# Performance work log

Hardware: AMD Instinct MI355X
Metric: run time of the kernel (lower is better)

The kernel has to match this reference:

```python
import jax, jax.numpy as jnp
import numpy as np
import math

S, B, H, NH, HD = 2048, 1, 4096, 32, 128
ROT = HD // 2  # 2D RoPE: each half of head_dim gets its own rotary embedding


def _rotate_half(x):
    x1, x2 = jnp.split(x, 2, axis=-1)
    return jnp.concatenate((-x2, x1), axis=-1)


def _rope_tables(max_pos, dim):
    inv_freq = 1.0 / (10000.0 ** (jnp.arange(0, dim, 2, dtype=jnp.float32) / dim))
    freqs = jnp.arange(max_pos, dtype=jnp.float32)[:, None] * inv_freq[None, :]  # [P, dim/2]
    emb = jnp.concatenate((freqs, freqs), axis=-1)  # [P, dim]
    return jnp.cos(emb), jnp.sin(emb)


def _apply_rope(q, k, cos_t, sin_t, pid):
    # q,k: [S,B,NH,ROT]; pid: [S,B]
    c = cos_t[pid][:, :, None, :]  # [S,B,1,ROT]
    s = sin_t[pid][:, :, None, :]
    return q * c + _rotate_half(q) * s, k * c + _rotate_half(k) * s


def setup_inputs() -> dict:
    key = jax.random.key(0)
    k1, k2, k3, k4, k5 = jax.random.split(key, 5)
    hidden_states = jax.random.normal(k1, (S, B, H), dtype=jnp.float32)
    pos = jnp.arange(S, dtype=jnp.int32)[None, :]          # [1,S] standard positions
    blk = jnp.zeros((1, S), dtype=jnp.int32)                # block positions (pre-gmask all zeros)
    position_ids = jnp.stack([pos, blk], axis=1)            # [B,2,S]
    # causal mask: True = masked out
    attention_mask = jnp.triu(jnp.ones((S, S), dtype=bool), k=1)[None, None]  # [B,1,S,S]
    Wqkv = jax.random.normal(k2, (3 * H, H), dtype=jnp.float32) * 0.02
    bqkv = jax.random.normal(k3, (3 * H,), dtype=jnp.float32) * 0.02
    Wd = jax.random.normal(k4, (H, H), dtype=jnp.float32) * 0.02
    bd = jax.random.normal(k5, (H,), dtype=jnp.float32) * 0.02
    return {"hidden_states": hidden_states, "position_ids": position_ids,
            "attention_mask": attention_mask, "layer_id": 5,
            "Wqkv": Wqkv, "bqkv": bqkv, "Wd": Wd, "bd": bd}


def reference(hidden_states, position_ids, attention_mask, layer_id, Wqkv, bqkv, Wd, bd):
    # QKV projection: [S,B,H] -> [S,B,NH,3*HD]
    mixed = hidden_states @ Wqkv.T + bqkv
    mixed = mixed.reshape(S, B, NH, 3 * HD)
    q, k, v = jnp.split(mixed, 3, axis=-1)  # each [S,B,NH,HD]

    # 2D rotary position embedding on the two head-dim halves
    q1, q2 = jnp.split(q, 2, axis=-1)
    k1, k2 = jnp.split(k, 2, axis=-1)
    cos_t, sin_t = _rope_tables(S, ROT)
    pid = position_ids[:, 0, :].T   # [S,B]
    bid = position_ids[:, 1, :].T   # [S,B]
    q1, k1 = _apply_rope(q1, k1, cos_t, sin_t, pid)
    q2, k2 = _apply_rope(q2, k2, cos_t, sin_t, bid)
    q = jnp.concatenate([q1, q2], axis=-1)
    k = jnp.concatenate([k1, k2], axis=-1)

    # layer-scaled attention scores
    coeff = float(layer_id + 1)
    q = q / (math.sqrt(HD) * coeff)
    scores = jnp.einsum('sbnd,tbnd->bnst', q, k)  # [B,NH,S,S]
    scores = jnp.where(attention_mask, jnp.float32(-10000.0), scores)
    scores = scores.astype(jnp.float32) * coeff
    probs = jax.nn.softmax(scores, axis=-1).astype(hidden_states.dtype)

    ctx = jnp.einsum('bnst,tbnd->sbnd', probs, v).reshape(S, B, NH * HD)
    return ctx @ Wd.T + bd  # [S,B,H]
```

## Files before the change

kernel.cpp:

```cpp
#include <hip/hip_runtime.h>


#define S_LEN 2048
#define NHEAD 32
#define HDIM 128
#define HID 4096

typedef float f32x4 __attribute__((ext_vector_type(4)));
typedef __bf16 bf16x8 __attribute__((ext_vector_type(8)));
typedef __bf16 bf16x4 __attribute__((ext_vector_type(4)));
typedef _Float16 f16x4 __attribute__((ext_vector_type(4)));
typedef _Float16 f16x8 __attribute__((ext_vector_type(8)));

__device__ __forceinline__ void gload16(const void* g, void* l) {
  __builtin_amdgcn_global_load_lds(
      (const __attribute__((address_space(1))) void*)g,
      (__attribute__((address_space(3))) void*)l, 16, 0, 0);
}

__global__ __launch_bounds__(256) void cvt_f32_bf16_kernel(
    const float* __restrict__ in, __bf16* __restrict__ out, int n4) {
  int i = blockIdx.x * 256 + threadIdx.x;
  if (i >= n4) return;
  f32x4 v = *(const f32x4*)(in + (size_t)i * 4);
  bf16x4 o;
  o[0] = (__bf16)v[0]; o[1] = (__bf16)v[1];
  o[2] = (__bf16)v[2]; o[3] = (__bf16)v[3];
  *(bf16x4*)(out + (size_t)i * 4) = o;
}

__device__ __forceinline__ void stage_half(const __bf16* __restrict__ G,
                                           int grow0, int Kstride, int kofs,
                                           __bf16* lds_half, int tid) {
#pragma unroll
  for (int i = 0; i < 2; ++i) {
    int idx = i * 512 + tid;
    int rr = idx >> 3;
    int offp = (idx & 7) * 16;
    int off = offp ^ ((rr & 7) << 4);
    const char* src =
        (const char*)(G + (size_t)(grow0 + rr) * Kstride + kofs) + off;
    char* dst = (char*)lds_half + idx * 16;
    gload16(src, dst);
  }
}

__device__ __forceinline__ bf16x8 ldsfrag(const __bf16* hb, int rowin, int ks,
                                          int lg) {
  int off = ((ks * 64 + lg * 16) ^ ((rowin & 7) << 4));
  return *(const bf16x8*)((const char*)hb + rowin * 128 + off);
}

template <int OUT_MODE>
__global__ __launch_bounds__(512, 2) void gemm256_kernel(
    const __bf16* __restrict__ A, const __bf16* __restrict__ B,
    const float* __restrict__ bias, void* __restrict__ Cout, int M, int N,
    int Kstride, int klen, int mtiles, int ksplit) {
  __shared__ __align__(16) __bf16 As[2][2][128 * 64];
  __shared__ __align__(16) __bf16 Bs[2][2][128 * 64];
  const int tid = threadIdx.x;
  int bid = blockIdx.x;
  int kh = 0;
  if (ksplit == 2) { kh = bid & 1; bid >>= 1; }
  const int kbase = kh * klen;
  int per_patch = mtiles * 8;
  int p = bid / per_patch, r = bid % per_patch;
  int mt = r % mtiles, nt = p * 8 + r / mtiles;
  int m0 = mt * 256, n0 = nt * 256;
  const int wid = tid >> 6, l = tid & 63;
  const int wm = wid >> 2, wn = wid & 3;
  const int lr = l & 15, lg = l >> 4;
  const int nk = klen >> 6;

  f32x4 acc[2][2][4][2];
#pragma unroll
  for (int a = 0; a < 2; ++a)
#pragma unroll
    for (int b = 0; b < 2; ++b)
#pragma unroll
      for (int c = 0; c < 4; ++c)
#pragma unroll
        for (int d = 0; d < 2; ++d) acc[a][b][c][d] = 0.f;

  stage_half(A, m0, Kstride, kbase, &As[0][0][0], tid);
  stage_half(A, m0 + 128, Kstride, kbase, &As[0][1][0], tid);
  stage_half(B, n0, Kstride, kbase, &Bs[0][0][0], tid);
  stage_half(B, n0 + 128, Kstride, kbase, &Bs[0][1][0], tid);
  if (nk > 1) {
    stage_half(A, m0, Kstride, kbase + 64, &As[1][0][0], tid);
    stage_half(B, n0, Kstride, kbase + 64, &Bs[1][0][0], tid);
    stage_half(B, n0 + 128, Kstride, kbase + 64, &Bs[1][1][0], tid);
    stage_half(A, m0 + 128, Kstride, kbase + 64, &As[1][1][0], tid);
    asm volatile("s_waitcnt vmcnt(8)" ::: "memory");
  } else {
    asm volatile("s_waitcnt vmcnt(0)" ::: "memory");
  }
  asm volatile("s_barrier" ::: "memory");

  for (int t = 0; t < nk; ++t) {
    const int cur = t & 1;
    const int kt2 = kbase + ((t + 2) << 6);
    const bool s2 = (t + 2 < nk);
    bf16x8 a[4][2], b0[2][2], b1[2][2];

#pragma unroll
    for (int mi = 0; mi < 4; ++mi)
#pragma unroll
      for (int ks = 0; ks < 2; ++ks)
        a[mi][ks] = ldsfrag(&As[cur][0][0], wm * 64 + mi * 16 + lr, ks, lg);
#pragma unroll
    for (int nj = 0; nj < 2; ++nj)
#pragma unroll
      for (int ks = 0; ks < 2; ++ks)
        b0[nj][ks] = ldsfrag(&Bs[cur][0][0], wn * 32 + nj * 16 + lr, ks, lg);
    __builtin_amdgcn_s_setprio(1);
#pragma unroll
    for (int mi = 0; mi < 4; ++mi)
#pragma unroll
      for (int nj = 0; nj < 2; ++nj)
#pragma unroll
        for (int ks = 0; ks < 2; ++ks)
          acc[0][0][mi][nj] = __builtin_amdgcn_mfma_f32_16x16x32_bf16(
              a[mi][ks], b0[nj][ks], acc[0][0][mi][nj], 0, 0, 0);
    __builtin_amdgcn_s_setprio(0);
    asm volatile("s_barrier" ::: "memory");

#pragma unroll
    for (int nj = 0; nj < 2; ++nj)
#pragma unroll
      for (int ks = 0; ks < 2; ++ks)
        b1[nj][ks] = ldsfrag(&Bs[cur][1][0], wn * 32 + nj * 16 + lr, ks, lg);
    if (s2) {
      stage_half(A, m0, Kstride, kt2, &As[cur][0][0], tid);
      stage_half(B, n0, Kstride, kt2, &Bs[cur][0][0], tid);
    }
    __builtin_amdgcn_s_setprio(1);
#pragma unroll
    for (int mi = 0; mi < 4; ++mi)
#pragma unroll
      for (int nj = 0; nj < 2; ++nj)
#pragma unroll
        for (int ks = 0; ks < 2; ++ks)
          acc[0][1][mi][nj] = __builtin_amdgcn_mfma_f32_16x16x32_bf16(
              a[mi][ks], b1[nj][ks], acc[0][1][mi][nj], 0, 0, 0);
    __builtin_amdgcn_s_setprio(0);
    asm volatile("s_barrier" ::: "memory");

#pragma unroll
    for (int mi = 0; mi < 4; ++mi)
#pragma unroll
      for (int ks = 0; ks < 2; ++ks)
        a[mi][ks] = ldsfrag(&As[cur][1][0], wm * 64 + mi * 16 + lr, ks, lg);
    if (s2) stage_half(B, n0 + 128, Kstride, kt2, &Bs[cur][1][0], tid);
    __builtin_amdgcn_s_setprio(1);
#pragma unroll
    for (int mi = 0; mi < 4; ++mi)
#pragma unroll
      for (int nj = 0; nj < 2; ++nj)
#pragma unroll
        for (int ks = 0; ks < 2; ++ks)
          acc[1][1][mi][nj] = __builtin_amdgcn_mfma_f32_16x16x32_bf16(
              a[mi][ks], b1[nj][ks], acc[1][1][mi][nj], 0, 0, 0);
    __builtin_amdgcn_s_setprio(0);
    asm volatile("s_barrier" ::: "memory");

    if (s2) stage_half(A, m0 + 128, Kstride, kt2, &As[cur][1][0], tid);
    __builtin_amdgcn_s_setprio(1);
#pragma unroll
    for (int mi = 0; mi < 4; ++mi)
#pragma unroll
      for (int nj = 0; nj < 2; ++nj)
#pragma unroll
        for (int ks = 0; ks < 2; ++ks)
          acc[1][0][mi][nj] = __builtin_amdgcn_mfma_f32_16x16x32_bf16(
              a[mi][ks], b0[nj][ks], acc[1][0][mi][nj], 0, 0, 0);
    __builtin_amdgcn_s_setprio(0);
    if (s2)
      asm volatile("s_waitcnt vmcnt(8)" ::: "memory");
    else
      asm volatile("s_waitcnt vmcnt(0)" ::: "memory");
    asm volatile("s_barrier" ::: "memory");
  }

  float* outF = (float*)Cout;
  if (OUT_MODE == 2) outF += (size_t)kh * M * N;
#pragma unroll
  for (int mh = 0; mh < 2; ++mh)
#pragma unroll
    for (int nh = 0; nh < 2; ++nh)
#pragma unroll
      for (int mi = 0; mi < 4; ++mi)
#pragma unroll
        for (int nj = 0; nj < 2; ++nj) {
          int row = m0 + mh * 128 + wm * 64 + mi * 16 + lg * 4;
          int col = n0 + nh * 128 + wn * 32 + nj * 16 + lr;
          float bv = (OUT_MODE == 2) ? 0.f : bias[col];
          f32x4 v = acc[mh][nh][mi][nj];
#pragma unroll
          for (int j = 0; j < 4; ++j) {
            float o = v[j] + bv;
            if (OUT_MODE == 1)
              ((__bf16*)Cout)[(size_t)(row + j) * N + col] = (__bf16)o;
            else
              outF[(size_t)(row + j) * N + col] = o;
          }
        }
}

__global__ __launch_bounds__(256) void reduce_addbias_kernel(
    const float* __restrict__ p0, const float* __restrict__ p1,
    const float* __restrict__ bias, float* __restrict__ out) {
  int i = blockIdx.x * 256 + threadIdx.x;
  int col = (i * 4) & (HID - 1);
  f32x4 a = *(const f32x4*)(p0 + (size_t)i * 4);
  f32x4 b = *(const f32x4*)(p1 + (size_t)i * 4);
  f32x4 c = *(const f32x4*)(bias + col);
  a = a + b + c;
  *(f32x4*)(out + (size_t)i * 4) = a;
}

__global__ __launch_bounds__(256) void rope_kernel(
    const __bf16* __restrict__ qkv, const int* __restrict__ pos_ids,
    __bf16* __restrict__ Q, __bf16* __restrict__ K, _Float16* __restrict__ VT) {
  int h = blockIdx.x & 31, sb = blockIdx.x >> 5;
  int s0 = sb * 64;
  int t = threadIdx.x;
  __shared__ float cs[64][2][2][32];
  __shared__ _Float16 vs[64][132];

  for (int idx = t; idx < 64 * 64; idx += 256) {
    int sl = idx >> 6, half = (idx >> 5) & 1, i = idx & 31;
    int p = pos_ids[half * S_LEN + s0 + sl];
    float f = powf(10000.f, -(float)i / 32.f);
    float ang = (float)p * f;
    cs[sl][half][0][i] = cosf(ang);
    cs[sl][half][1][i] = sinf(ang);
  }
#pragma unroll
  for (int c = 0; c < 4; c++) {
    int chunk = c * 256 + t;
    int slv = chunk >> 4, co = (chunk & 15) * 8;
    const __bf16* vsrc =
        qkv + (size_t)(s0 + slv) * (NHEAD * 3 * HDIM) + h * 384 + 256 + co;
    bf16x8 vv = *(const bf16x8*)vsrc;
    f16x4 a, b;
#pragma unroll
    for (int j = 0; j < 4; j++) {
      a[j] = (_Float16)(float)vv[j];
      b[j] = (_Float16)(float)vv[4 + j];
    }
    *(f16x4*)&vs[slv][co] = a;
    *(f16x4*)&vs[slv][co + 4] = b;
  }
  __syncthreads();

  {
    int sl = t >> 2, role = t & 3;
    int isK = role >> 1, half = role & 1;
    const __bf16* src = qkv + (size_t)(s0 + sl) * (NHEAD * 3 * HDIM) + h * 384 +
                        isK * 128 + half * 64;
    float scale = isK ? 1.f : 0.08838834764831845f;
    float x[64];
    bf16x8 buf[8];
#pragma unroll
    for (int c = 0; c < 8; c++) buf[c] = *(const bf16x8*)(src + c * 8);
#pragma unroll
    for (int c = 0; c < 8; c++)
#pragma unroll
      for (int j = 0; j < 8; j++) x[c * 8 + j] = (float)buf[c][j];
    bf16x8 ob[8];
#pragma unroll
    for (int i = 0; i < 64; i++) {
      int ii = i & 31;
      float cv = cs[sl][half][0][ii], sv = cs[sl][half][1][ii];
      float partner = (i < 32) ? x[i + 32] : x[i - 32];
      float sgn = (i < 32) ? -1.f : 1.f;
      float o = (x[i] * cv + sgn * partner * sv) * scale;
      ob[i >> 3][i & 7] = (__bf16)o;
    }
    __bf16* dst = (isK ? K : Q) + ((size_t)h * S_LEN + s0 + sl) * HDIM + half * 64;
#pragma unroll
    for (int c = 0; c < 8; c++) *(bf16x8*)(dst + c * 8) = ob[c];
  }

#pragma unroll
  for (int c = 0; c < 4; c++) {
    int chunk = c * 256 + t;
    int d = chunk >> 3, so = (chunk & 7) * 8;
    f16x8 o;
#pragma unroll
    for (int j = 0; j < 8; j++) o[j] = vs[so + j][d];
    *(f16x8*)(VT + ((size_t)h * HDIM + d) * S_LEN + s0 + so) = o;
  }
}

__global__ __launch_bounds__(256, 2) void attn_kernel(
    const __bf16* __restrict__ Q, const __bf16* __restrict__ K,
    const _Float16* __restrict__ VT, __bf16* __restrict__ ctx) {
  int b = blockIdx.x;
  int h = b & 31;
  int qb = 15 - (b >> 5);
  int w = threadIdx.x >> 6, l = threadIdx.x & 63;
  int lr = l & 15, lg = l >> 4;
  int q0 = qb * 128 + w * 32;
  const __bf16* Qh = Q + (size_t)h * S_LEN * HDIM;
  const __bf16* Kh = K + (size_t)h * S_LEN * HDIM;
  const _Float16* Vh = VT + (size_t)h * HDIM * S_LEN;

  bf16x8 qfA[4], qfB[4];
#pragma unroll
  for (int kk = 0; kk < 4; kk++) {
    qfA[kk] = *(const bf16x8*)(Qh + (size_t)(q0 + lr) * HDIM + kk * 32 + lg * 8);
    qfB[kk] =
        *(const bf16x8*)(Qh + (size_t)(q0 + 16 + lr) * HDIM + kk * 32 + lg * 8);
  }

  f32x4 accA[8], accB[8];
#pragma unroll
  for (int tt = 0; tt < 8; tt++) { accA[tt] = 0.f; accB[tt] = 0.f; }
  float mA = -INFINITY, lsA = 0.f, mB = -INFINITY, lsB = 0.f;
  int qgA = q0 + lr, qgB = q0 + 16 + lr;
  int qmax = q0 + 31;

  for (int kv0 = 0; kv0 <= qmax; kv0 += 16) {
    f32x4 stA = 0.f, stB = 0.f;
#pragma unroll
    for (int kk = 0; kk < 4; kk++) {
      bf16x8 kf =
          *(const bf16x8*)(Kh + (size_t)(kv0 + lr) * HDIM + kk * 32 + lg * 8);
      stA = __builtin_amdgcn_mfma_f32_16x16x32_bf16(kf, qfA[kk], stA, 0, 0, 0);
      stB = __builtin_amdgcn_mfma_f32_16x16x32_bf16(kf, qfB[kk], stB, 0, 0, 0);
    }
    float tmA = -INFINITY, tmB = -INFINITY;
#pragma unroll
    for (int j = 0; j < 4; j++) {
      int kvg = kv0 + lg * 4 + j;
      if (kvg > qgA) stA[j] = -INFINITY;
      if (kvg > qgB) stB[j] = -INFINITY;
      tmA = fmaxf(tmA, stA[j]);
      tmB = fmaxf(tmB, stB[j]);
    }
    tmA = fmaxf(tmA, __shfl_xor(tmA, 16));
    tmA = fmaxf(tmA, __shfl_xor(tmA, 32));
    tmB = fmaxf(tmB, __shfl_xor(tmB, 16));
    tmB = fmaxf(tmB, __shfl_xor(tmB, 32));
    int need = __any((tmA > mA) || (tmB > mB));
    float mnA = fmaxf(mA, tmA), mnB = fmaxf(mB, tmB);

    f16x4 paA, paB;
    float tsA = 0.f, tsB = 0.f;
#pragma unroll
    for (int j = 0; j < 4; j++) {
      float pA = __expf(stA[j] - mnA);
      float pB = __expf(stB[j] - mnB);
      tsA += pA; tsB += pB;
      paA[j] = (_Float16)pA; paB[j] = (_Float16)pB;
    }
    tsA += __shfl_xor(tsA, 16);
    tsA += __shfl_xor(tsA, 32);
    tsB += __shfl_xor(tsB, 16);
    tsB += __shfl_xor(tsB, 32);

    if (need) {
      float scA = __expf(mA - mnA), scB = __expf(mB - mnB);
      lsA = lsA * scA + tsA;
      lsB = lsB * scB + tsB;
      float sAj[4], sBj[4];
#pragma unroll
      for (int j = 0; j < 4; j++) {
        sAj[j] = __shfl(scA, lg * 4 + j);
        sBj[j] = __shfl(scB, lg * 4 + j);
      }
#pragma unroll
      for (int tt = 0; tt < 8; tt++)
#pragma unroll
        for (int j = 0; j < 4; j++) {
          accA[tt][j] *= sAj[j];
          accB[tt][j] *= sBj[j];
        }
    } else {
      lsA += tsA;
      lsB += tsB;
    }
    mA = mnA; mB = mnB;

#pragma unroll
    for (int tt = 0; tt < 8; tt++) {
      f16x4 vb =
          *(const f16x4*)(Vh + (size_t)(tt * 16 + lr) * S_LEN + kv0 + lg * 4);
      accA[tt] = __builtin_amdgcn_mfma_f32_16x16x16f16(paA, vb, accA[tt], 0, 0, 0);
      accB[tt] = __builtin_amdgcn_mfma_f32_16x16x16f16(paB, vb, accB[tt], 0, 0, 0);
    }
  }

  float rA[4], rB[4];
#pragma unroll
  for (int j = 0; j < 4; j++) {
    rA[j] = 1.f / __shfl(lsA, lg * 4 + j);
    rB[j] = 1.f / __shfl(lsB, lg * 4 + j);
  }
#pragma unroll
  for (int tt = 0; tt < 8; tt++) {
#pragma unroll
    for (int j = 0; j < 4; j++) {
      int qoA = q0 + lg * 4 + j;
      int qoB = q0 + 16 + lg * 4 + j;
      ctx[(size_t)qoA * (NHEAD * HDIM) + h * HDIM + tt * 16 + lr] =
          (__bf16)(accA[tt][j] * rA[j]);
      ctx[(size_t)qoB * (NHEAD * HDIM) + h * HDIM + tt * 16 + lr] =
          (__bf16)(accB[tt][j] * rB[j]);
    }
  }
}

extern "C" void kernel_launch(void* const* d_in, const int* in_sizes, int n_in,
                              void* d_out, int out_size, void* d_ws,
                              size_t ws_size, hipStream_t stream) {
  const float* hs = (const float*)d_in[0];
  const int* pos_ids = (const int*)d_in[1];
  const float* Wqkv = (const float*)d_in[4];
  const float* bqkv = (const float*)d_in[5];
  const float* Wd = (const float*)d_in[6];
  const float* bd = (const float*)d_in[7];
  float* out = (float*)d_out;

  char* ws = (char*)d_ws;
  constexpr size_t OFF_W = 16777216ULL;
  constexpr size_t OFF_QKV = OFF_W + 100663296ULL;
  constexpr size_t OFF_Q = OFF_QKV + 50331648ULL;
  constexpr size_t OFF_K = OFF_Q + 16777216ULL;
  constexpr size_t OFF_V = OFF_K + 16777216ULL;
  __bf16* hsb = (__bf16*)(ws);
  __bf16* wqkvb = (__bf16*)(ws + OFF_W);
  __bf16* wdb = (__bf16*)(ws + OFF_W);
  float* pk = (float*)(ws + OFF_W + 33554432ULL);
  __bf16* qkvb = (__bf16*)(ws + OFF_QKV);
  __bf16* ctxb = qkvb;
  __bf16* Qb = (__bf16*)(ws + OFF_Q);
  __bf16* Kb = (__bf16*)(ws + OFF_K);
  _Float16* Vtb = (_Float16*)(ws + OFF_V);

  cvt_f32_bf16_kernel<<<(S_LEN * HID) / 4 / 256, 256, 0, stream>>>(
      hs, hsb, S_LEN * HID / 4);
  cvt_f32_bf16_kernel<<<(3 * HID * HID) / 4 / 256, 256, 0, stream>>>(
      Wqkv, wqkvb, 3 * HID * HID / 4);

  gemm256_kernel<1><<<8 * 48, 512, 0, stream>>>(hsb, wqkvb, bqkv, qkvb, S_LEN,
                                                3 * HID, HID, HID, 8, 1);

  cvt_f32_bf16_kernel<<<(HID * HID) / 4 / 256, 256, 0, stream>>>(
      Wd, wdb, HID * HID / 4);

  rope_kernel<<<NHEAD * (S_LEN / 64), 256, 0, stream>>>(qkvb, pos_ids, Qb, Kb,
                                                        Vtb);

  attn_kernel<<<NHEAD * (S_LEN / 128), 256, 0, stream>>>(Qb, Kb, Vtb, ctxb);

  gemm256_kernel<2><<<2 * 8 * 16, 512, 0, stream>>>(ctxb, wdb, bd, pk, S_LEN,
                                                    HID, HID, HID / 2, 8, 2);
  reduce_addbias_kernel<<<(S_LEN * HID) / 4 / 256, 256, 0, stream>>>(
      pk, pk + (size_t)S_LEN * HID, bd, out);
}
```

Measured before the change: 683.7 us.

## Software-pipeline LDS fragment reads across k-steps in 256x256 GEMM mainloop

Restructures the GEMM mainloop so LDS fragment loads for the next quarter-step (and the next k-tile's A/B0 fragments) are issued before the current MFMA block, using ping-pong register sets and a 2x unrolled loop. The intent is to hide LDS read latency behind MFMA work and shift waitcnt placement (vmcnt 6) earlier. It removes the nk==1 fallback in the prologue and assumes nk is even, and increases register pressure with extra fragment buffers.

Result: slower. 1.355 ms (+98.2%).

```diff
diff --git a/kernel.cpp b/kernel.cpp
--- a/kernel.cpp
+++ b/kernel.cpp
@@ -50,6 +50,61 @@
   int off = ((ks * 64 + lg * 16) ^ ((rowin & 7) << 4));
   return *(const bf16x8*)((const char*)hb + rowin * 128 + off);
 }
+
+#define READ_A(DST, SLOT)                                                     \
+  _Pragma("unroll") for (int mi = 0; mi < 4; ++mi)                            \
+      _Pragma("unroll") for (int ks = 0; ks < 2; ++ks) DST[mi][ks] =          \
+      ldsfrag(SLOT, wm * 64 + mi * 16 + lr, ks, lg);
+
+#define READ_B(DST, SLOT)                                                     \
+  _Pragma("unroll") for (int nj = 0; nj < 2; ++nj)                            \
+      _Pragma("unroll") for (int ks = 0; ks < 2; ++ks) DST[nj][ks] =          \
+      ldsfrag(SLOT, wn * 32 + nj * 16 + lr, ks, lg);
+
+#define MFMA_Q(MH, NH, AFR, BFR)                                              \
+  __builtin_amdgcn_s_setprio(1);                                              \
+  _Pragma("unroll") for (int mi = 0; mi < 4; ++mi)                            \
+      _Pragma("unroll") for (int nj = 0; nj < 2; ++nj)                        \
+          _Pragma("unroll") for (int ks = 0; ks < 2; ++ks)                    \
+              acc[MH][NH][mi][nj] =                                           \
+      __builtin_amdgcn_mfma_f32_16x16x32_bf16(AFR[mi][ks], BFR[nj][ks],       \
+                                              acc[MH][NH][mi][nj], 0, 0, 0);  \
+  __builtin_amdgcn_s_setprio(0);
+
+#define GITER(CUR, B0C, B0N, T)                                               \
+  {                                                                           \
+    const int kt2 = kbase + ((T) + 2) * 64;                                   \
+    const bool s2 = ((T) + 2 < nk);                                           \
+    const bool s1 = ((T) + 1 < nk);                                           \
+                                                \
+    READ_B(b1, &Bs[CUR][1][0]);                                               \
+    MFMA_Q(0, 0, aP, B0C);                                                    \
+    asm volatile("s_barrier" ::: "memory");                                   \
+                              \
+    if (s2) {                                                                 \
+      stage_half(A, m0, Kstride, kt2, &As[CUR][0][0], tid);                   \
+      stage_half(B, n0, Kstride, kt2, &Bs[CUR][0][0], tid);                   \
+    }                                                                         \
+    READ_A(aQ, &As[CUR][1][0]);                                               \
+    MFMA_Q(0, 1, aP, b1);                                                     \
+    asm volatile("s_barrier" ::: "memory");                                   \
+                   \
+    if (s2) stage_half(B, n0 + 128, Kstride, kt2, &Bs[CUR][1][0], tid);       \
+    MFMA_Q(1, 1, aQ, b1);                                                     \
+    if (s2)                                                                   \
+      asm volatile("s_waitcnt vmcnt(6)" ::: "memory");                        \
+    else                                                                      \
+      asm volatile("s_waitcnt vmcnt(0)" ::: "memory");                        \
+    asm volatile("s_barrier" ::: "memory");                                   \
+                        \
+    if (s2) stage_half(A, m0 + 128, Kstride, kt2, &As[CUR][1][0], tid);       \
+    if (s1) {                                                                 \
+      READ_A(aP, &As[(CUR) ^ 1][0][0]);                                       \
+      READ_B(B0N, &Bs[(CUR) ^ 1][0][0]);                                      \
+    }                                                                         \
+    MFMA_Q(1, 0, aQ, B0C);                                                    \
+    asm volatile("s_barrier" ::: "memory");                                   \
+  }
 
 template <int OUT_MODE>
 __global__ __launch_bounds__(512, 2) void gemm256_kernel(
@@ -82,104 +137,24 @@
 #pragma unroll
         for (int d = 0; d < 2; ++d) acc[a][b][c][d] = 0.f;
 
+  bf16x8 aP[4][2], aQ[4][2], b0A[2][2], b0B[2][2], b1[2][2];
+
   stage_half(A, m0, Kstride, kbase, &As[0][0][0], tid);
-  stage_half(A, m0 + 128, Kstride, kbase, &As[0][1][0], tid);
   stage_half(B, n0, Kstride, kbase, &Bs[0][0][0], tid);
   stage_half(B, n0 + 128, Kstride, kbase, &Bs[0][1][0], tid);
-  if (nk > 1) {
-    stage_half(A, m0, Kstride, kbase + 64, &As[1][0][0], tid);
-    stage_half(B, n0, Kstride, kbase + 64, &Bs[1][0][0], tid);
-    stage_half(B, n0 + 128, Kstride, kbase + 64, &Bs[1][1][0], tid);
-    stage_half(A, m0 + 128, Kstride, kbase + 64, &As[1][1][0], tid);
-    asm volatile("s_waitcnt vmcnt(8)" ::: "memory");
-  } else {
-    asm volatile("s_waitcnt vmcnt(0)" ::: "memory");
-  }
+  stage_half(A, m0 + 128, Kstride, kbase, &As[0][1][0], tid);
+  stage_half(A, m0, Kstride, kbase + 64, &As[1][0][0], tid);
+  stage_half(B, n0, Kstride, kbase + 64, &Bs[1][0][0], tid);
+  stage_half(B, n0 + 128, Kstride, kbase + 64, &Bs[1][1][0], tid);
+  stage_half(A, m0 + 128, Kstride, kbase + 64, &As[1][1][0], tid);
+  asm volatile("s_waitcnt vmcnt(8)" ::: "memory");
   asm volatile("s_barrier" ::: "memory");
-
-  for (int t = 0; t < nk; ++t) {
-    const int cur = t & 1;
-    const int kt2 = kbase + ((t + 2) << 6);
-    const bool s2 = (t + 2 < nk);
-    bf16x8 a[4][2], b0[2][2], b1[2][2];
-
-#pragma unroll
-    for (int mi = 0; mi < 4; ++mi)
-#pragma unroll
-      for (int ks = 0; ks < 2; ++ks)
-        a[mi][ks] = ldsfrag(&As[cur][0][0], wm * 64 + mi * 16 + lr, ks, lg);
-#pragma unroll
-    for (int nj = 0; nj < 2; ++nj)
-#pragma unroll
-      for (int ks = 0; ks < 2; ++ks)
-        b0[nj][ks] = ldsfrag(&Bs[cur][0][0], wn * 32 + nj * 16 + lr, ks, lg);
-    __builtin_amdgcn_s_setprio(1);
-#pragma unroll
-    for (int mi = 0; mi < 4; ++mi)
-#pragma unroll
-      for (int nj = 0; nj < 2; ++nj)
-#pragma unroll
-        for (int ks = 0; ks < 2; ++ks)
-          acc[0][0][mi][nj] = __builtin_amdgcn_mfma_f32_16x16x32_bf16(
-              a[mi][ks], b0[nj][ks], acc[0][0][mi][nj], 0, 0, 0);
-    __builtin_amdgcn_s_setprio(0);
-    asm volatile("s_barrier" ::: "memory");
-
-#pragma unroll
-    for (int nj = 0; nj < 2; ++nj)
-#pragma unroll
-      for (int ks = 0; ks < 2; ++ks)
-        b1[nj][ks] = ldsfrag(&Bs[cur][1][0], wn * 32 + nj * 16 + lr, ks, lg);
-    if (s2) {
-      stage_half(A, m0, Kstride, kt2, &As[cur][0][0], tid);
-      stage_half(B, n0, Kstride, kt2, &Bs[cur][0][0], tid);
-    }
-    __builtin_amdgcn_s_setprio(1);
-#pragma unroll
-    for (int mi = 0; mi < 4; ++mi)
-#pragma unroll
-      for (int nj = 0; nj < 2; ++nj)
-#pragma unroll
-        for (int ks = 0; ks < 2; ++ks)
-          acc[0][1][mi][nj] = __builtin_amdgcn_mfma_f32_16x16x32_bf16(
-              a[mi][ks], b1[nj][ks], acc[0][1][mi][nj], 0, 0, 0);
-    __builtin_amdgcn_s_setprio(0);
-    asm volatile("s_barrier" ::: "memory");
-
-#pragma unroll
-    for (int mi = 0; mi < 4; ++mi)
-#pragma unroll
-      for (int ks = 0; ks < 2; ++ks)
-        a[mi][ks] = ldsfrag(&As[cur][1][0], wm * 64 + mi * 16 + lr, ks, lg);
-    if (s2) stage_half(B, n0 + 128, Kstride, kt2, &Bs[cur][1][0], tid);
-    __builtin_amdgcn_s_setprio(1);
-#pragma unroll
-    for (int mi = 0; mi < 4; ++mi)
-#pragma unroll
-      for (int nj = 0; nj < 2; ++nj)
-#pragma unroll
-        for (int ks = 0; ks < 2; ++ks)
-          acc[1][1][mi][nj] = __builtin_amdgcn_mfma_f32_16x16x32_bf16(
-              a[mi][ks], b1[nj][ks], acc[1][1][mi][nj], 0, 0, 0);
-    __builtin_amdgcn_s_setprio(0);
-    asm volatile("s_barrier" ::: "memory");
-
-    if (s2) stage_half(A, m0 + 128, Kstride, kt2, &As[cur][1][0], tid);
-    __builtin_amdgcn_s_setprio(1);
-#pragma unroll
-    for (int mi = 0; mi < 4; ++mi)
-#pragma unroll
-      for (int nj = 0; nj < 2; ++nj)
-#pragma unroll
-        for (int ks = 0; ks < 2; ++ks)
-          acc[1][0][mi][nj] = __builtin_amdgcn_mfma_f32_16x16x32_bf16(
-              a[mi][ks], b0[nj][ks], acc[1][0][mi][nj], 0, 0, 0);
-    __builtin_amdgcn_s_setprio(0);
-    if (s2)
-      asm volatile("s_waitcnt vmcnt(8)" ::: "memory");
-    else
-      asm volatile("s_waitcnt vmcnt(0)" ::: "memory");
-    asm volatile("s_barrier" ::: "memory");
+  READ_A(aP, &As[0][0][0]);
+  READ_B(b0A, &Bs[0][0][0]);
+
+  for (int t = 0; t < nk; t += 2) {
+    GITER(0, b0A, b0B, t)
+    GITER(1, b0B, b0A, t + 1)
   }
 
   float* outF = (float*)Cout;
```
